# Optimization experiments

Hardware: AMD Instinct MI355X
Metric: run time of the kernel (lower is better)

## Reference

```python
import jax, jax.numpy as jnp
import numpy as np

D_MODEL, D_INNER, D_STATE, DT_RANK, D_CONV = 192, 384, 16, 12, 4
DEPTH, HP, NHEADS, BATCH = 24, 14, 3, 4
EPS = 1e-5

def _make_rope():
    half = D_MODEL // 2
    fb = 1.0 / (10000.0 ** (np.arange(0, half, 2, dtype=np.float64) / half))
    t = np.arange(HP, dtype=np.float64)
    fr = np.repeat(np.outer(t, fb), 2, axis=-1)  # [14, 96]
    f = np.concatenate([np.broadcast_to(fr[:, None, :], (HP, HP, half)),
                        np.broadcast_to(fr[None, :, :], (HP, HP, half))], -1).reshape(HP * HP, D_MODEL)
    return jnp.asarray(np.cos(f), jnp.float32), jnp.asarray(np.sin(f), jnp.float32)

ROPE_COS, ROPE_SIN = _make_rope()

def _rotate_half(x):
    a, b = x[..., 0::2], x[..., 1::2]
    return jnp.stack([-b, a], axis=-1).reshape(x.shape)

def _apply_rope(h):
    # odd token count: cls token at position 0 is skipped (Vim behavior)
    sp = h[:, 1:, :]
    sp = sp * ROPE_COS + _rotate_half(sp) * ROPE_SIN
    return jnp.concatenate([h[:, :1, :], sp], axis=1)

def _rmsnorm(x, w):
    return x * jax.lax.rsqrt(jnp.mean(x * x, axis=-1, keepdims=True) + EPS) * w

def _scan_dir(u, z, cw, cb, xw, dw, db, alog, dp):
    # u, z: [B, L, d_inner]
    B, L, d = u.shape
    up = jnp.pad(u, ((0, 0), (D_CONV - 1, 0), (0, 0)))  # causal left pad
    xc = cb + sum(up[:, k:k + L, :] * cw[:, k] for k in range(D_CONV))
    x = jax.nn.silu(xc)
    dbl = x @ xw.T  # [B, L, dt_rank + 2*d_state]
    dt = dbl[..., :DT_RANK]
    Bm = dbl[..., DT_RANK:DT_RANK + D_STATE]
    C = dbl[..., DT_RANK + D_STATE:]
    delta = jax.nn.softplus(dt @ dw.T + db)  # [B, L, d]
    A = -jnp.exp(alog)  # [d, N]
    dA = jnp.exp(jnp.einsum('bld,dn->bldn', delta, A))
    dBu = jnp.einsum('bld,bln->bldn', delta * x, Bm)
    def step(h, inp):
        dA_t, dBu_t, C_t = inp
        h = dA_t * h + dBu_t
        return h, jnp.einsum('bdn,bn->bd', h, C_t)
    h0 = jnp.zeros((B, d, D_STATE), u.dtype)
    _, ys = jax.lax.scan(step, h0, (jnp.swapaxes(dA, 0, 1), jnp.swapaxes(dBu, 0, 1), jnp.swapaxes(C, 0, 1)))
    y = jnp.swapaxes(ys, 0, 1) + x * dp
    return y * jax.nn.silu(z)

def _mamba_bi(h, lp):
    nw, iw, cw, cb, xw, dw, db, alog, dp, ow = lp
    xz = h @ iw.T  # [B, L, 2*d_inner]
    x, z = xz[..., :D_INNER], xz[..., D_INNER:]
    yf = _scan_dir(x, z, cw[0], cb[0], xw[0], dw[0], db[0], alog[0], dp[0])
    yb = _scan_dir(x[:, ::-1], z[:, ::-1], cw[1], cb[1], xw[1], dw[1], db[1], alog[1], dp[1])[:, ::-1]
    return ((yf + yb) @ ow.T) * 0.5  # if_devide_out=True

def _encoder(img, pw_, pb_, cls_, pos_, nw, iw, cw, cb, xw, dw, db, alog, dp, ow, nfw):
    B = img.shape[0]
    p = jax.lax.conv_general_dilated(img, pw_, (16, 16), 'VALID',
            dimension_numbers=('NCHW', 'OIHW', 'NCHW')) + pb_[None, :, None, None]
    tok = jnp.transpose(p.reshape(B, D_MODEL, HP * HP), (0, 2, 1))
    cls = jnp.broadcast_to(cls_[None, None, :], (B, 1, D_MODEL))
    h = jnp.concatenate([cls, tok], axis=1) + pos_
    def layer(carry, lp):
        hs, res = carry
        hs = _apply_rope(hs)
        res = hs + res  # fused add-norm, prenorm
        hs = _rmsnorm(res, lp[0])
        hs = _mamba_bi(hs, lp)
        return (hs, res), None
    (h, res), _ = jax.lax.scan(layer, (h, jnp.zeros_like(h)), (nw, iw, cw, cb, xw, dw, db, alog, dp, ow))
    h = _rmsnorm(h + res, nfw)  # final fused add-norm
    return jnp.transpose(h[:, 1:, :].reshape(B, HP, HP, D_MODEL), (0, 3, 1, 2))

def _dwconv3(x, w):
    return jax.lax.conv_general_dilated(x, w[:, None, :, :], (1, 1), 'SAME',
            dimension_numbers=('NCHW', 'OIHW', 'NCHW'), feature_group_count=D_MODEL)

def _cross_attention(qi, ki, vi, qw, qdw, kw, kdw, vw, vdw, pw, temp):
    q = _dwconv3(jnp.einsum('bchw,oc->bohw', qi, qw), qdw)
    k = _dwconv3(jnp.einsum('bchw,oc->bohw', ki, kw), kdw)
    v = _dwconv3(jnp.einsum('bchw,oc->bohw', vi, vw), vdw)
    B, C, H, W = q.shape
    c = C // NHEADS
    qh = q.reshape(B, NHEADS, c, H * W)
    kh = k.reshape(B, NHEADS, c, H * W)
    vh = v.reshape(B, NHEADS, c, H * W)
    qh = qh / jnp.maximum(jnp.linalg.norm(qh, axis=-1, keepdims=True), 1e-12)
    kh = kh / jnp.maximum(jnp.linalg.norm(kh, axis=-1, keepdims=True), 1e-12)
    attn = jax.nn.softmax(jnp.einsum('bhcn,bhdn->bhcd', qh, kh) * temp, axis=-1)
    out = jnp.einsum('bhcd,bhdn->bhcn', attn, vh).reshape(B, C, H, W)
    return jnp.einsum('bchw,oc->bohw', out, pw)

def setup_inputs() -> dict:
    key = jax.random.key(0)
    ks = jax.random.split(key, 24)
    r = lambda k, s, sc=0.02: sc * jax.random.normal(k, s, dtype=jnp.float32)
    return {
        'x1': jax.random.normal(ks[0], (BATCH, 3, 224, 224), dtype=jnp.float32),
        'x2': jax.random.normal(ks[1], (BATCH, 3, 224, 224), dtype=jnp.float32),
        'patch_w': r(ks[2], (2, D_MODEL, 3, 16, 16)),
        'patch_b': jnp.zeros((2, D_MODEL), jnp.float32),
        'cls_tok': r(ks[3], (2, D_MODEL)),
        'pos_embed': r(ks[4], (2, HP * HP + 1, D_MODEL)),
        'norm_w': jnp.ones((2, DEPTH, D_MODEL), jnp.float32),
        'in_w': r(ks[5], (2, DEPTH, 2 * D_INNER, D_MODEL)),
        'conv_w': r(ks[6], (2, DEPTH, 2, D_INNER, D_CONV), 0.2),
        'conv_b': jnp.zeros((2, DEPTH, 2, D_INNER), jnp.float32),
        'xp_w': r(ks[7], (2, DEPTH, 2, DT_RANK + 2 * D_STATE, D_INNER)),
        'dt_w': r(ks[8], (2, DEPTH, 2, D_INNER, DT_RANK), 0.1),
        'dt_b': jnp.log(jnp.expm1(jax.random.uniform(ks[9], (2, DEPTH, 2, D_INNER), jnp.float32, 1e-3, 0.1))),
        'A_log': jnp.asarray(jnp.broadcast_to(jnp.log(jnp.arange(1.0, D_STATE + 1.0, dtype=jnp.float32)), (2, DEPTH, 2, D_INNER, D_STATE))),
        'Dp': jnp.ones((2, DEPTH, 2, D_INNER), jnp.float32),
        'out_w': r(ks[10], (2, DEPTH, D_MODEL, D_INNER)),
        'normf_w': jnp.ones((2, D_MODEL), jnp.float32),
        'qw': r(ks[11], (D_MODEL, D_MODEL)),
        'qdw': r(ks[12], (D_MODEL, 3, 3), 0.2),
        'kw': r(ks[13], (D_MODEL, D_MODEL)),
        'kdw': r(ks[14], (D_MODEL, 3, 3), 0.2),
        'vw': r(ks[15], (D_MODEL, D_MODEL)),
        'vdw': r(ks[16], (D_MODEL, 3, 3), 0.2),
        'pw': r(ks[17], (D_MODEL, D_MODEL)),
        'temp': jnp.ones((NHEADS, 1, 1), jnp.float32),
    }

def reference(x1, x2, patch_w, patch_b, cls_tok, pos_embed, norm_w, in_w, conv_w, conv_b, xp_w, dt_w, dt_b, A_log, Dp, out_w, normf_w, qw, qdw, kw, kdw, vw, vdw, pw, temp):
    f1 = _encoder(x1, patch_w[0], patch_b[0], cls_tok[0], pos_embed[0], norm_w[0], in_w[0], conv_w[0], conv_b[0], xp_w[0], dt_w[0], dt_b[0], A_log[0], Dp[0], out_w[0], normf_w[0])
    f2 = _encoder(x2, patch_w[1], patch_b[1], cls_tok[1], pos_embed[1], norm_w[1], in_w[1], conv_w[1], conv_b[1], xp_w[1], dt_w[1], dt_b[1], A_log[1], Dp[1], out_w[1], normf_w[1])
    return _cross_attention(f1, f2, f2, qw, qdw, kw, kdw, vw, vdw, pw, temp)
```

## Files before the change

kernel.cpp:

```cpp
#include <hip/hip_runtime.h>

#define DM 192
#define DI 384
#define DSt 16
#define DTR 12
#define DC 4
#define NL 24
#define HP 14
#define NH 3
#define NB 4
#define SL 197
#define NT 196
#define XZW 768
#define DBLW 44
#define SEG 50

static __device__ __forceinline__ float siluf(float x) { return x / (1.f + expf(-x)); }
static __device__ __forceinline__ float softplusf(float x) { return (x > 20.f) ? x : log1pf(expf(x)); }

template <int CTRL>
static __device__ __forceinline__ float dpp_addf(float x) {
  int y = __builtin_amdgcn_update_dpp(0, __float_as_int(x), CTRL, 0xF, 0xF, true);
  return x + __int_as_float(y);
}

static __device__ __forceinline__ float blk_sum3(float v, float* wsum) {
  for (int off = 32; off; off >>= 1) v += __shfl_xor(v, off, 64);
  int wid = threadIdx.x >> 6;
  if ((threadIdx.x & 63) == 0) wsum[wid] = v;
  __syncthreads();
  return wsum[0] + wsum[1] + wsum[2];
}
static __device__ __forceinline__ float blk_sum4(float v, float* wsum) {
  for (int off = 32; off; off >>= 1) v += __shfl_xor(v, off, 64);
  int wid = threadIdx.x >> 6;
  if ((threadIdx.x & 63) == 0) wsum[wid] = v;
  __syncthreads();
  return wsum[0] + wsum[1] + wsum[2] + wsum[3];
}

__global__ void k_rope_init(float* __restrict__ cosT, float* __restrict__ sinT) {
  int gid = blockIdx.x * blockDim.x + threadIdx.x;
  if (gid >= NT * DM) return;
  int c = gid % DM, tk = gid / DM;
  int py = tk / HP, px = tk % HP;
  int pos = (c < 96) ? py : px;
  int i = (c < 96) ? (c >> 1) : ((c - 96) >> 1);
  double fb = pow(10000.0, -((double)(2 * i)) / 96.0);
  double ang = (double)pos * fb;
  cosT[gid] = (float)cos(ang);
  sinT[gid] = (float)sin(ang);
}

__global__ void k_im2col(const float* __restrict__ x1, const float* __restrict__ x2,
                         float* __restrict__ P) {
  int gid = blockIdx.x * blockDim.x + threadIdx.x;
  if (gid >= 2 * 784 * 768) return;
  int col = gid % 768;
  int row = (gid / 768) % 784;
  int e = gid / (768 * 784);
  int b = row / NT, tk = row % NT;
  int c = col >> 8, r = (col >> 4) & 15, xx = col & 15;
  int py = tk / HP, px = tk % HP;
  const float* img = e ? x2 : x1;
  P[gid] = img[((size_t)(b * 3 + c) * 224 + (py * 16 + r)) * 224 + (px * 16 + xx)];
}

__global__ void k_patch_fin(const float* __restrict__ pm, const float* __restrict__ pb,
                            const float* __restrict__ cls, const float* __restrict__ pos,
                            float* __restrict__ h, float* __restrict__ res) {
  int gid = blockIdx.x * blockDim.x + threadIdx.x;
  if (gid >= 2 * NB * SL * DM) return;
  int c = gid % DM;
  int t = (gid / DM) % SL;
  int b = (gid / (DM * SL)) % NB;
  int e = gid / (DM * SL * NB);
  float v;
  if (t == 0) v = cls[e * DM + c];
  else v = pm[((size_t)e * 784 + b * NT + (t - 1)) * DM + c] + pb[e * DM + c];
  h[gid] = v + pos[((size_t)e * SL + t) * DM + c];
  res[gid] = 0.f;
}

__global__ __launch_bounds__(DM) void k_rope_res_norm(
    const float* __restrict__ h, float* __restrict__ res, float* __restrict__ hs,
    const float* __restrict__ nw, const float* __restrict__ cosT,
    const float* __restrict__ sinT, int l) {
  int bx = blockIdx.x;
  int t = bx % SL; int b = (bx / SL) % NB; int e = bx / (SL * NB);
  int c = threadIdx.x;
  __shared__ float sh[DM];
  __shared__ float wsum[3];
  size_t base = ((size_t)(e * NB + b) * SL + t) * DM;
  sh[c] = h[base + c];
  __syncthreads();
  float v = sh[c];
  if (t > 0) {
    int tk = t - 1;
    float co = cosT[tk * DM + c], si = sinT[tk * DM + c];
    float partner = sh[c ^ 1];
    float rot = (c & 1) ? partner : -partner;
    v = v * co + rot * si;
  }
  float r = res[base + c] + v;
  res[base + c] = r;
  float tot = blk_sum3(r * r, wsum);
  float scale = rsqrtf(tot / (float)DM + 1e-5f);
  hs[base + c] = r * scale * nw[(size_t)(e * NL + l) * DM + c];
}

struct MM4 {
  const float* A0[4];
  const float* A1[4];
  const float* B[4];
  float* C[4];
};
__global__ __launch_bounds__(256) void k_mm32(MM4 p, int M, int N, int K, float alpha) {
  const float* __restrict__ A0 = p.A0[blockIdx.z];
  const float* __restrict__ A1 = p.A1[blockIdx.z];
  const float* __restrict__ Bw = p.B[blockIdx.z];
  float* __restrict__ C = p.C[blockIdx.z];
  __shared__ __align__(16) float As[16][34];
  __shared__ __align__(16) float Bs[16][68];
  int tid = threadIdx.x;
  int m0 = blockIdx.y * 32, n0 = blockIdx.x * 64;
  int tm = tid >> 4, tn = tid & 15;
  int srow = tid >> 2, skq = tid & 3;
  int srowA = (tid & 127) >> 2;
  bool doA = tid < 128;
  int gmA = min(m0 + srowA, M - 1);
  int gnB = min(n0 + srow, N - 1);
  bool hasA1 = (A1 != nullptr);
  float4 ra, rb, ra1;

  auto GLOAD = [&](int k0) {
    if (doA) {
      ra = *(const float4*)&A0[(size_t)gmA * K + k0 + skq * 4];
      if (hasA1) ra1 = *(const float4*)&A1[(size_t)gmA * K + k0 + skq * 4];
    }
    rb = *(const float4*)&Bw[(size_t)gnB * K + k0 + skq * 4];
  };
  auto DSW = [&]() {
    int kb = skq * 4;
    if (doA) {
      float av0 = ra.x, av1 = ra.y, av2 = ra.z, av3 = ra.w;
      if (hasA1) { av0 += ra1.x; av1 += ra1.y; av2 += ra1.z; av3 += ra1.w; }
      As[kb + 0][srowA] = av0;
      As[kb + 1][srowA] = av1;
      As[kb + 2][srowA] = av2;
      As[kb + 3][srowA] = av3;
    }
    Bs[kb + 0][srow] = rb.x;
    Bs[kb + 1][srow] = rb.y;
    Bs[kb + 2][srow] = rb.z;
    Bs[kb + 3][srow] = rb.w;
  };

  float acc[2][4] = {};
  int T = K >> 4;
  GLOAD(0);
  DSW();
  __syncthreads();
#pragma unroll 1
  for (int kt = 1; kt <= T; ++kt) {
    if (kt < T) GLOAD(kt * 16);
#pragma unroll
    for (int kk = 0; kk < 16; ++kk) {
      float2 a = *(const float2*)&As[kk][tm * 2];
      float4 b = *(const float4*)&Bs[kk][tn * 4];
      acc[0][0] += a.x * b.x; acc[0][1] += a.x * b.y;
      acc[0][2] += a.x * b.z; acc[0][3] += a.x * b.w;
      acc[1][0] += a.y * b.x; acc[1][1] += a.y * b.y;
      acc[1][2] += a.y * b.z; acc[1][3] += a.y * b.w;
    }
    if (kt < T) {
      __syncthreads();
      DSW();
      __syncthreads();
    }
  }
#pragma unroll
  for (int mi = 0; mi < 2; ++mi) {
    int gm = m0 + tm * 2 + mi;
    if (gm >= M) continue;
    int gn = n0 + tn * 4;
    if (gn + 3 < N) {
      float4 o4 = make_float4(alpha * acc[mi][0], alpha * acc[mi][1],
                              alpha * acc[mi][2], alpha * acc[mi][3]);
      *(float4*)&C[(size_t)gm * N + gn] = o4;
    } else {
#pragma unroll
      for (int ni = 0; ni < 4; ++ni)
        if (gn + ni < N) C[(size_t)gm * N + gn + ni] = alpha * acc[mi][ni];
    }
  }
}

__global__ void k_conv_silu(const float* __restrict__ xz, const float* __restrict__ cw,
                            const float* __restrict__ cb, float* __restrict__ xs, int l) {
  int gid = blockIdx.x * blockDim.x + threadIdx.x;
  if (gid >= 2 * 2 * NB * SL * DI) return;
  int d = gid % DI;
  int t = (gid / DI) % SL;
  int b = (gid / (DI * SL)) % NB;
  int dir = (gid / (DI * SL * NB)) % 2;
  int e = gid / (DI * SL * NB * 2);
  size_t pidx = (size_t)(e * NL + l) * 2 + dir;
  const float* cwp = cw + (pidx * DI + d) * DC;
  float acc = cb[pidx * DI + d];
#pragma unroll
  for (int k = 0; k < DC; ++k) {
    int ts = t - (DC - 1) + k;
    if (ts >= 0) {
      int torig = dir ? (SL - 1 - ts) : ts;
      acc += cwp[k] * xz[((size_t)(e * NB + b) * SL + torig) * XZW + d];
    }
  }
  xs[gid] = siluf(acc);
}

__global__ void k_delta(const float* __restrict__ dbl, const float* __restrict__ dtw,
                        const float* __restrict__ dtb, float* __restrict__ delta, int l) {
  int gid = blockIdx.x * blockDim.x + threadIdx.x;
  if (gid >= 2 * 2 * NB * SL * DI) return;
  int d = gid % DI;
  int t = (gid / DI) % SL;
  int b = (gid / (DI * SL)) % NB;
  int dir = (gid / (DI * SL * NB)) % 2;
  int e = gid / (DI * SL * NB * 2);
  int z = e * 2 + dir;
  size_t pidx = (size_t)(e * NL + l) * 2 + dir;
  const float* row = dbl + ((size_t)(z * NB + b) * SL + t) * DBLW;
  const float* w = dtw + (pidx * DI + d) * DTR;
  float acc = dtb[pidx * DI + d];
#pragma unroll
  for (int r = 0; r < DTR; ++r) acc += row[r] * w[r];
  delta[gid] = softplusf(acc);
}

__global__ __launch_bounds__(256) void k_scan(
    const float* __restrict__ xs, const float* __restrict__ delta,
    const float* __restrict__ dbl, const float* __restrict__ xz,
    const float* __restrict__ alog, const float* __restrict__ dpw,
    float* __restrict__ y0, float* __restrict__ y1, int l) {
  int bx = blockIdx.x;
  int g4 = bx % (DI / 4);
  int b = (bx / (DI / 4)) % NB;
  int dir = (bx / (DI / 4 * NB)) % 2;
  int e = bx / (DI / 4 * NB * 2);
  int tid = threadIdx.x;
  int w = tid >> 6;
  int lane = tid & 63;
  int n = lane & 15;
  int chl = lane >> 4;
  int d = g4 * 4 + chl;
  size_t pidx = (size_t)(e * NL + l) * 2 + dir;
  float A = -expf(alog[(pidx * DI + d) * DSt + n]);
  float dpv = dpw[pidx * DI + d];
  int z = e * 2 + dir;
  size_t gdbase = ((size_t)(z * NB + b) * SL) * DI + d;
  size_t dblbase = ((size_t)(z * NB + b) * SL) * DBLW;
  size_t gzbase = ((size_t)(e * NB + b) * SL) * XZW + DI + d;
  float* yout = dir ? y1 : y0;
  size_t ybase = ((size_t)(e * NB + b) * SL) * DI + d;

  int t0 = w * SEG;
  int t1 = min(SL, t0 + SEG);

  float h = 0.f, ap = 1.f;
#pragma unroll 2
  for (int t = t0; t < t1; ++t) {
    float dv = delta[gdbase + (size_t)t * DI];
    float xv = xs[gdbase + (size_t)t * DI];
    float bm = dbl[dblbase + (size_t)t * DBLW + DTR + n];
    float a = __expf(dv * A);
    h = a * h + (dv * xv) * bm;
    ap *= a;
  }

  __shared__ float sh_h[4][64];
  __shared__ float sh_a[4][64];
  sh_h[w][lane] = h;
  sh_a[w][lane] = ap;
  __syncthreads();
  float hin = 0.f;
#pragma unroll
  for (int j = 0; j < 3; ++j)
    if (j < w) hin = sh_a[j][lane] * hin + sh_h[j][lane];

  h = hin;
#pragma unroll 2
  for (int t = t0; t < t1; ++t) {
    float dv = delta[gdbase + (size_t)t * DI];
    float xv = xs[gdbase + (size_t)t * DI];
    float bm = dbl[dblbase + (size_t)t * DBLW + DTR + n];
    float cv = dbl[dblbase + (size_t)t * DBLW + DTR + DSt + n];
    float a = __expf(dv * A);
    h = a * h + (dv * xv) * bm;
    float pc = h * cv;
    pc = dpp_addf<0xB1>(pc);
    pc = dpp_addf<0x4E>(pc);
    pc = dpp_addf<0x114>(pc);
    pc = dpp_addf<0x118>(pc);
    if (n == 15) {
      int torig = dir ? (SL - 1 - t) : t;
      float zv = xz[gzbase + (size_t)torig * XZW];
      float yv = pc + xv * dpv;
      yout[ybase + (size_t)torig * DI] = yv * siluf(zv);
    }
  }
}

__global__ __launch_bounds__(DM) void k_final_norm(
    const float* __restrict__ h, const float* __restrict__ res,
    const float* __restrict__ nfw, float* __restrict__ fT) {
  int bx = blockIdx.x;
  int tk = bx % NT; int b = (bx / NT) % NB; int e = bx / (NT * NB);
  int c = threadIdx.x;
  __shared__ float wsum[3];
  size_t base = ((size_t)(e * NB + b) * SL + (tk + 1)) * DM;
  float r = h[base + c] + res[base + c];
  float tot = blk_sum3(r * r, wsum);
  float scale = rsqrtf(tot / (float)DM + 1e-5f);
  fT[((size_t)(e * NB + b) * NT + tk) * DM + c] = r * scale * nfw[e * DM + c];
}

__global__ void k_dwconv(const float* __restrict__ qkvl, const float* __restrict__ qdw,
                         const float* __restrict__ kdw, const float* __restrict__ vdw,
                         float* __restrict__ qkvd) {
  int gid = blockIdx.x * blockDim.x + threadIdx.x;
  if (gid >= 3 * NB * DM * NT) return;
  int nn = gid % NT;
  int o = (gid / NT) % DM;
  int b = (gid / (NT * DM)) % NB;
  int zz = gid / (NT * DM * NB);
  const float* wsel = (zz == 0 ? qdw : (zz == 1 ? kdw : vdw)) + o * 9;
  int y = nn / HP, x = nn % HP;
  const float* in = qkvl + ((size_t)zz * NB + b) * NT * DM;
  float acc = 0.f;
#pragma unroll
  for (int ky = 0; ky < 3; ++ky) {
    int yy = y + ky - 1;
    if (yy < 0 || yy >= HP) continue;
#pragma unroll
    for (int kx = 0; kx < 3; ++kx) {
      int xx = x + kx - 1;
      if (xx < 0 || xx >= HP) continue;
      acc += in[(size_t)(yy * HP + xx) * DM + o] * wsel[ky * 3 + kx];
    }
  }
  qkvd[gid] = acc;
}

__global__ __launch_bounds__(256) void k_l2norm(float* __restrict__ qkvd) {
  int bx = blockIdx.x;
  int C = bx % DM; int b = (bx / DM) % NB; int zz = bx / (DM * NB);
  int i = threadIdx.x;
  __shared__ float wsum[4];
  float* row = qkvd + ((size_t)zz * NB + b) * DM * NT + (size_t)C * NT;
  float v = (i < NT) ? row[i] : 0.f;
  float tot = blk_sum4(v * v, wsum);
  float sc = 1.f / fmaxf(sqrtf(tot), 1e-12f);
  if (i < NT) row[i] = v * sc;
}

__global__ __launch_bounds__(64) void k_attn_sm(const float* __restrict__ qkvd,
                                                const float* __restrict__ temp,
                                                float* __restrict__ P) {
  int bx = blockIdx.x;
  int i = bx % 64; int hh = (bx / 64) % NH; int b = bx / (64 * NH);
  int j = threadIdx.x;
  __shared__ float qs[NT];
  const float* qrow = qkvd + ((size_t)0 * NB + b) * DM * NT + (size_t)(hh * 64 + i) * NT;
  for (int k = j; k < NT; k += 64) qs[k] = qrow[k];
  __syncthreads();
  const float* krow = qkvd + ((size_t)1 * NB + b) * DM * NT + (size_t)(hh * 64 + j) * NT;
  float acc = 0.f;
  for (int k = 0; k < NT; ++k) acc += qs[k] * krow[k];
  acc *= temp[hh];
  float m = acc;
  for (int off = 32; off; off >>= 1) m = fmaxf(m, __shfl_xor(m, off, 64));
  float ex = expf(acc - m);
  float s = ex;
  for (int off = 32; off; off >>= 1) s += __shfl_xor(s, off, 64);
  P[((size_t)(b * NH + hh) * 64 + i) * 64 + j] = ex / s;
}

__global__ __launch_bounds__(256) void k_av(const float* __restrict__ P,
                                            const float* __restrict__ qkvd,
                                            float* __restrict__ att) {
  int bx = blockIdx.x;
  int i = bx % 64; int hh = (bx / 64) % NH; int b = bx / (64 * NH);
  int nn = threadIdx.x;
  __shared__ float ps[64];
  if (nn < 64) ps[nn] = P[((size_t)(b * NH + hh) * 64 + i) * 64 + nn];
  __syncthreads();
  if (nn >= NT) return;
  const float* vbase = qkvd + ((size_t)2 * NB + b) * DM * NT + (size_t)(hh * 64) * NT + nn;
  float acc = 0.f;
  for (int j = 0; j < 64; ++j) acc += ps[j] * vbase[(size_t)j * NT];
  att[((size_t)b * DM + hh * 64 + i) * NT + nn] = acc;
}

__global__ __launch_bounds__(256) void k_out(const float* __restrict__ att,
                                             const float* __restrict__ pw,
                                             float* __restrict__ out) {
  int bx = blockIdx.x;
  int o = bx % DM; int b = bx / DM;
  int nn = threadIdx.x;
  if (nn >= NT) return;
  const float* abase = att + (size_t)b * DM * NT + nn;
  const float* w = pw + (size_t)o * DM;
  float acc = 0.f;
  for (int c = 0; c < DM; ++c) acc += abase[(size_t)c * NT] * w[c];
  out[((size_t)b * DM + o) * NT + nn] = acc;
}

extern "C" void kernel_launch(void* const* d_in, const int* in_sizes, int n_in,
                              void* d_out, int out_size, void* d_ws, size_t ws_size,
                              hipStream_t stream) {
  const float* x1      = (const float*)d_in[0];
  const float* x2      = (const float*)d_in[1];
  const float* patch_w = (const float*)d_in[2];
  const float* patch_b = (const float*)d_in[3];
  const float* cls_tok = (const float*)d_in[4];
  const float* pos_emb = (const float*)d_in[5];
  const float* norm_w  = (const float*)d_in[6];
  const float* in_w    = (const float*)d_in[7];
  const float* conv_w  = (const float*)d_in[8];
  const float* conv_b  = (const float*)d_in[9];
  const float* xp_w    = (const float*)d_in[10];
  const float* dt_w    = (const float*)d_in[11];
  const float* dt_b    = (const float*)d_in[12];
  const float* A_log   = (const float*)d_in[13];
  const float* Dp      = (const float*)d_in[14];
  const float* out_w   = (const float*)d_in[15];
  const float* normf_w = (const float*)d_in[16];
  const float* qw      = (const float*)d_in[17];
  const float* qdw     = (const float*)d_in[18];
  const float* kw      = (const float*)d_in[19];
  const float* kdw     = (const float*)d_in[20];
  const float* vw      = (const float*)d_in[21];
  const float* vdw     = (const float*)d_in[22];
  const float* pww     = (const float*)d_in[23];
  const float* temp    = (const float*)d_in[24];

  float* ws = (float*)d_ws;
  size_t o = 0;
  float* cosT = ws + o; o += (size_t)NT * DM;
  float* sinT = ws + o; o += (size_t)NT * DM;
  float* hB   = ws + o; o += 2ull * NB * SL * DM;
  float* resB = ws + o; o += 2ull * NB * SL * DM;
  float* hsB  = ws + o; o += 2ull * NB * SL * DM;
  float* xzB  = ws + o; o += 2ull * NB * SL * XZW;
  float* xsB  = ws + o; o += 4ull * NB * SL * DI;
  float* dblB = ws + o; o += 4ull * NB * SL * DBLW;
  float* delB = ws + o; o += 4ull * NB * SL * DI;
  float* y0B  = ws + o; o += 2ull * NB * SL * DI;
  float* y1B  = ws + o; o += 2ull * NB * SL * DI;
  float* fTB  = ws + o; o += 2ull * NB * NT * DM;
  float* qkvL = ws + o; o += 3ull * NB * NT * DM;
  float* qkvD = ws + o; o += 3ull * NB * DM * NT;
  float* Pb   = ws + o; o += (size_t)NB * NH * 64 * 64;
  float* attB = ws + o; o += (size_t)NB * DM * NT;
  (void)ws_size; (void)in_sizes; (void)n_in; (void)out_size;

  const int M = NB * SL;

  k_rope_init<<<(NT * DM + 255) / 256, 256, 0, stream>>>(cosT, sinT);

  float* Pm = delB;
  float* Pout = y0B;
  k_im2col<<<(2 * 784 * 768 + 255) / 256, 256, 0, stream>>>(x1, x2, Pm);
  {
    MM4 p{};
    for (int e = 0; e < 2; ++e) {
      p.A0[e] = Pm + (size_t)e * 784 * 768;
      p.A1[e] = nullptr;
      p.B[e]  = patch_w + (size_t)e * DM * 768;
      p.C[e]  = Pout + (size_t)e * 784 * DM;
    }
    dim3 g((DM + 63) / 64, (784 + 31) / 32, 2);
    k_mm32<<<g, 256, 0, stream>>>(p, 784, DM, 768, 1.f);
  }
  k_patch_fin<<<(2 * NB * SL * DM + 255) / 256, 256, 0, stream>>>(
      Pout, patch_b, cls_tok, pos_emb, hB, resB);

  for (int l = 0; l < NL; ++l) {
    k_rope_res_norm<<<2 * NB * SL, DM, 0, stream>>>(hB, resB, hsB, norm_w, cosT, sinT, l);

    {
      MM4 p{};
      for (int e = 0; e < 2; ++e) {
        p.A0[e] = hsB + (size_t)e * M * DM;
        p.A1[e] = nullptr;
        p.B[e]  = in_w + (size_t)(e * NL + l) * XZW * DM;
        p.C[e]  = xzB + (size_t)e * M * XZW;
      }
      dim3 g((XZW + 63) / 64, (M + 31) / 32, 2);
      k_mm32<<<g, 256, 0, stream>>>(p, M, XZW, DM, 1.f);
    }

    k_conv_silu<<<(2 * 2 * NB * SL * DI + 255) / 256, 256, 0, stream>>>(xzB, conv_w, conv_b, xsB, l);

    {
      MM4 p{};
      for (int z = 0; z < 4; ++z) {
        int e = z / 2, dir = z % 2;
        p.A0[z] = xsB + (size_t)z * M * DI;
        p.A1[z] = nullptr;
        p.B[z]  = xp_w + ((size_t)(e * NL + l) * 2 + dir) * DBLW * DI;
        p.C[z]  = dblB + (size_t)z * M * DBLW;
      }
      dim3 g((DBLW + 63) / 64, (M + 31) / 32, 4);
      k_mm32<<<g, 256, 0, stream>>>(p, M, DBLW, DI, 1.f);
    }

    k_delta<<<(2 * 2 * NB * SL * DI + 255) / 256, 256, 0, stream>>>(dblB, dt_w, dt_b, delB, l);

    k_scan<<<2 * 2 * NB * (DI / 4), 256, 0, stream>>>(xsB, delB, dblB, xzB, A_log, Dp, y0B, y1B, l);

    {
      MM4 p{};
      for (int e = 0; e < 2; ++e) {
        p.A0[e] = y0B + (size_t)e * M * DI;
        p.A1[e] = y1B + (size_t)e * M * DI;
        p.B[e]  = out_w + (size_t)(e * NL + l) * DM * DI;
        p.C[e]  = hB + (size_t)e * M * DM;
      }
      dim3 g((DM + 63) / 64, (M + 31) / 32, 2);
      k_mm32<<<g, 256, 0, stream>>>(p, M, DM, DI, 0.5f);
    }
  }

  k_final_norm<<<2 * NB * NT, DM, 0, stream>>>(hB, resB, normf_w, fTB);

  {
    MM4 p{};
    const int Mq = NB * NT;
    p.A0[0] = fTB;                         p.A1[0] = nullptr; p.B[0] = qw; p.C[0] = qkvL;
    p.A0[1] = fTB + (size_t)NB * NT * DM;  p.A1[1] = nullptr; p.B[1] = kw; p.C[1] = qkvL + (size_t)Mq * DM;
    p.A0[2] = fTB + (size_t)NB * NT * DM;  p.A1[2] = nullptr; p.B[2] = vw; p.C[2] = qkvL + 2ull * Mq * DM;
    dim3 g((DM + 63) / 64, (Mq + 31) / 32, 3);
    k_mm32<<<g, 256, 0, stream>>>(p, Mq, DM, DM, 1.f);
  }

  k_dwconv<<<(3 * NB * DM * NT + 255) / 256, 256, 0, stream>>>(qkvL, qdw, kdw, vdw, qkvD);
  k_l2norm<<<2 * NB * DM, 256, 0, stream>>>(qkvD);
  k_attn_sm<<<NB * NH * 64, 64, 0, stream>>>(qkvD, temp, Pb);
  k_av<<<NB * NH * 64, 256, 0, stream>>>(Pb, qkvD, attB);
  k_out<<<NB * DM, 256, 0, stream>>>(attB, pww, (float*)d_out);
}
```

Measured before the change: 3.435 ms.

## Restructure selective scan to four states per thread with eight time segments

Each thread in the Mamba scan kernel now carries four SSM states, loaded with float4 vector loads, instead of one. A wave therefore covers 16 channels instead of 4, and each block runs 8 time segments of 25 steps across 512 threads instead of 4 segments of 50. The C-reduction over states shrinks from a 16-lane DPP tree to a local 4-term sum plus a 4-lane DPP reduce. The aim is to cut redundant per-channel loads and shorten the serial chain per wave. The cost is fewer, larger blocks and a longer cross-segment carry step, which may reduce occupancy.

```diff
diff --git a/kernel.cpp b/kernel.cpp
--- a/kernel.cpp
+++ b/kernel.cpp
@@ -13,7 +13,8 @@
 #define NT 196
 #define XZW 768
 #define DBLW 44
-#define SEG 50
+#define NSEG 8
+#define SEGL 25
 
 static __device__ __forceinline__ float siluf(float x) { return x / (1.f + expf(-x)); }
 static __device__ __forceinline__ float softplusf(float x) { return (x > 20.f) ? x : log1pf(expf(x)); }
@@ -238,24 +239,25 @@
   delta[gid] = softplusf(acc);
 }
 
-__global__ __launch_bounds__(256) void k_scan(
+__global__ __launch_bounds__(512) void k_scan(
     const float* __restrict__ xs, const float* __restrict__ delta,
     const float* __restrict__ dbl, const float* __restrict__ xz,
     const float* __restrict__ alog, const float* __restrict__ dpw,
     float* __restrict__ y0, float* __restrict__ y1, int l) {
   int bx = blockIdx.x;
-  int g4 = bx % (DI / 4);
-  int b = (bx / (DI / 4)) % NB;
-  int dir = (bx / (DI / 4 * NB)) % 2;
-  int e = bx / (DI / 4 * NB * 2);
+  int dg = bx % (DI / 16);
+  int b = (bx / (DI / 16)) % NB;
+  int dir = (bx / (DI / 16 * NB)) % 2;
+  int e = bx / (DI / 16 * NB * 2);
   int tid = threadIdx.x;
   int w = tid >> 6;
   int lane = tid & 63;
-  int n = lane & 15;
-  int chl = lane >> 4;
-  int d = g4 * 4 + chl;
+  int ch = lane >> 2;
+  int st4 = lane & 3;
+  int d = dg * 16 + ch;
   size_t pidx = (size_t)(e * NL + l) * 2 + dir;
-  float A = -expf(alog[(pidx * DI + d) * DSt + n]);
+  float4 a4 = *(const float4*)&alog[((size_t)(pidx * DI + d)) * DSt + st4 * 4];
+  float A0 = -expf(a4.x), A1 = -expf(a4.y), A2 = -expf(a4.z), A3 = -expf(a4.w);
   float dpv = dpw[pidx * DI + d];
   int z = e * 2 + dir;
   size_t gdbase = ((size_t)(z * NB + b) * SL) * DI + d;
@@ -264,45 +266,61 @@
   float* yout = dir ? y1 : y0;
   size_t ybase = ((size_t)(e * NB + b) * SL) * DI + d;
 
-  int t0 = w * SEG;
-  int t1 = min(SL, t0 + SEG);
-
-  float h = 0.f, ap = 1.f;
-#pragma unroll 2
+  int t0 = w * SEGL;
+  int t1 = min(SL, t0 + SEGL);
+
+  float h0 = 0.f, h1 = 0.f, h2 = 0.f, h3 = 0.f;
+  float p0 = 1.f, p1 = 1.f, p2 = 1.f, p3 = 1.f;
+#pragma unroll 1
   for (int t = t0; t < t1; ++t) {
     float dv = delta[gdbase + (size_t)t * DI];
     float xv = xs[gdbase + (size_t)t * DI];
-    float bm = dbl[dblbase + (size_t)t * DBLW + DTR + n];
-    float a = __expf(dv * A);
-    h = a * h + (dv * xv) * bm;
-    ap *= a;
-  }
-
-  __shared__ float sh_h[4][64];
-  __shared__ float sh_a[4][64];
-  sh_h[w][lane] = h;
-  sh_a[w][lane] = ap;
-  __syncthreads();
-  float hin = 0.f;
-#pragma unroll
-  for (int j = 0; j < 3; ++j)
-    if (j < w) hin = sh_a[j][lane] * hin + sh_h[j][lane];
-
-  h = hin;
-#pragma unroll 2
+    float4 bm = *(const float4*)&dbl[dblbase + (size_t)t * DBLW + DTR + st4 * 4];
+    float dvxv = dv * xv;
+    float e0 = __expf(dv * A0), e1 = __expf(dv * A1);
+    float e2 = __expf(dv * A2), e3 = __expf(dv * A3);
+    h0 = e0 * h0 + dvxv * bm.x; p0 *= e0;
+    h1 = e1 * h1 + dvxv * bm.y; p1 *= e1;
+    h2 = e2 * h2 + dvxv * bm.z; p2 *= e2;
+    h3 = e3 * h3 + dvxv * bm.w; p3 *= e3;
+  }
+
+  __shared__ __align__(16) float4 sh_h[NSEG][64];
+  __shared__ __align__(16) float4 sh_a[NSEG][64];
+  sh_h[w][lane] = make_float4(h0, h1, h2, h3);
+  sh_a[w][lane] = make_float4(p0, p1, p2, p3);
+  __syncthreads();
+  float i0 = 0.f, i1 = 0.f, i2 = 0.f, i3 = 0.f;
+#pragma unroll
+  for (int j = 0; j < NSEG - 1; ++j) {
+    if (j < w) {
+      float4 hh = sh_h[j][lane];
+      float4 aa = sh_a[j][lane];
+      i0 = aa.x * i0 + hh.x;
+      i1 = aa.y * i1 + hh.y;
+      i2 = aa.z * i2 + hh.z;
+      i3 = aa.w * i3 + hh.w;
+    }
+  }
+
+  h0 = i0; h1 = i1; h2 = i2; h3 = i3;
+#pragma unroll 1
   for (int t = t0; t < t1; ++t) {
     float dv = delta[gdbase + (size_t)t * DI];
     float xv = xs[gdbase + (size_t)t * DI];
-    float bm = dbl[dblbase + (size_t)t * DBLW + DTR + n];
-    float cv = dbl[dblbase + (size_t)t * DBLW + DTR + DSt + n];
-    float a = __expf(dv * A);
-    h = a * h + (dv * xv) * bm;
-    float pc = h * cv;
+    float4 bm = *(const float4*)&dbl[dblbase + (size_t)t * DBLW + DTR + st4 * 4];
+    float4 cv = *(const float4*)&dbl[dblbase + (size_t)t * DBLW + DTR + DSt + st4 * 4];
+    float dvxv = dv * xv;
+    float e0 = __expf(dv * A0), e1 = __expf(dv * A1);
+    float e2 = __expf(dv * A2), e3 = __expf(dv * A3);
+    h0 = e0 * h0 + dvxv * bm.x;
+    h1 = e1 * h1 + dvxv * bm.y;
+    h2 = e2 * h2 + dvxv * bm.z;
+    h3 = e3 * h3 + dvxv * bm.w;
+    float pc = h0 * cv.x + h1 * cv.y + h2 * cv.z + h3 * cv.w;
     pc = dpp_addf<0xB1>(pc);
     pc = dpp_addf<0x4E>(pc);
-    pc = dpp_addf<0x114>(pc);
-    pc = dpp_addf<0x118>(pc);
-    if (n == 15) {
+    if (st4 == 0) {
       int torig = dir ? (SL - 1 - t) : t;
       float zv = xz[gzbase + (size_t)torig * XZW];
       float yv = pc + xv * dpv;
@@ -518,7 +536,7 @@
 
     k_delta<<<(2 * 2 * NB * SL * DI + 255) / 256, 256, 0, stream>>>(dblB, dt_w, dt_b, delB, l);
 
-    k_scan<<<2 * 2 * NB * (DI / 4), 256, 0, stream>>>(xsB, delB, dblB, xzB, A_log, Dp, y0B, y1B, l);
+    k_scan<<<2 * 2 * NB * (DI / 16), 512, 0, stream>>>(xsB, delB, dblB, xzB, A_log, Dp, y0B, y1B, l);
 
     {
       MM4 p{};
```

Result: faster. 2.853 ms (-16.9%).
